# Optimization experiments

Hardware: AMD Instinct MI355X
Metric: run time of the kernel (lower is better)

Reference implementation:

```python
import jax, jax.numpy as jnp
import numpy as np

B, S, E, H = 4, 2048, 1024, 16
HD = E // H  # head_dim = 64


def setup_inputs() -> dict:
    key = jax.random.key(0)
    ks = jax.random.split(key, 9)
    s_in = 1.0 / np.sqrt(E)
    return {
        "x": jax.random.normal(ks[0], (B, S, E), dtype=jnp.float32),
        "Wq": jax.random.normal(ks[1], (E, E), dtype=jnp.float32) * s_in,
        "bq": jax.random.normal(ks[2], (E,), dtype=jnp.float32) * 0.01,
        "Wk": jax.random.normal(ks[3], (E, E), dtype=jnp.float32) * s_in,
        "bk": jax.random.normal(ks[4], (E,), dtype=jnp.float32) * 0.01,
        "Wv": jax.random.normal(ks[5], (E, E), dtype=jnp.float32) * s_in,
        "bv": jax.random.normal(ks[6], (E,), dtype=jnp.float32) * 0.01,
        "Wo": jax.random.normal(ks[7], (E, E), dtype=jnp.float32) * s_in,
        "bo": jax.random.normal(ks[8], (E,), dtype=jnp.float32) * 0.01,
    }


def reference(x, Wq, bq, Wk, bk, Wv, bv, Wo, bo):
    b, s, e = x.shape
    # fused QKV projections (equivalent to concatenated per-head linears)
    q = x @ Wq + bq  # [b, s, e]
    k = x @ Wk + bk
    v = x @ Wv + bv
    # split heads: [b, h, s, hd]
    def split(t):
        return t.reshape(b, s, H, HD).transpose(0, 2, 1, 3)
    q, k, v = split(q), split(k), split(v)
    scale = 1.0 / np.sqrt(HD)
    attn = jnp.einsum("bhqd,bhkd->bhqk", q, k) * scale  # [b, h, s, s]
    causal = jnp.tril(jnp.ones((s, s), dtype=bool))
    attn = jnp.where(causal[None, None], attn, -jnp.inf)
    attn = jax.nn.softmax(attn, axis=-1)
    y = jnp.einsum("bhqk,bhkd->bhqd", attn, v)  # [b, h, s, hd]
    y = y.transpose(0, 2, 1, 3).reshape(b, s, e)
    return y @ Wo + bo
```

## Files before the change

### kernel.cpp

```cpp
#include <hip/hip_runtime.h>
#include <hip/hip_bf16.h>

#define B_ 4
#define S_ 2048
#define E_ 1024
#define H_ 16
#define HD_ 64
#define QS 3072

typedef __attribute__((ext_vector_type(8))) short bf16x8;
typedef __attribute__((ext_vector_type(4))) float f32x4;

__device__ __forceinline__ float b2f(unsigned short u) {
    union { unsigned u; float f; } v; v.u = ((unsigned)u) << 16; return v.f;
}
__device__ __forceinline__ unsigned short f2b(float f) {
    union { float f; unsigned u; } v; v.f = f;
    unsigned lsb = (v.u >> 16) & 1u;
    v.u += 0x7fffu + lsb;
    return (unsigned short)(v.u >> 16);
}
__device__ __forceinline__ unsigned cvtpk_bf16(float lo, float hi) {
    unsigned r;
    asm("v_cvt_pk_bf16_f32 %0, %1, %2" : "=v"(r) : "v"(lo), "v"(hi));
    return r;
}

typedef const __attribute__((address_space(1))) unsigned glb_u32;
typedef __attribute__((address_space(3))) unsigned lds_u32;
__device__ __forceinline__ void gl_lds16(const unsigned short* g,
                                         unsigned short* l) {
    __builtin_amdgcn_global_load_lds((glb_u32*)g, (lds_u32*)l, 16, 0, 0);
}

__global__ void cvt_f32_to_bf16(const float* __restrict__ in,
                                unsigned short* __restrict__ out, int n8) {
    int i = blockIdx.x * blockDim.x + threadIdx.x;
    if (i >= n8) return;
    const float4* p = (const float4*)(in + (size_t)i * 8);
    float4 a = p[0], b = p[1];
    bf16x8 o;
    o[0] = (short)f2b(a.x); o[1] = (short)f2b(a.y);
    o[2] = (short)f2b(a.z); o[3] = (short)f2b(a.w);
    o[4] = (short)f2b(b.x); o[5] = (short)f2b(b.y);
    o[6] = (short)f2b(b.z); o[7] = (short)f2b(b.w);
    *(bf16x8*)(out + (size_t)i * 8) = o;
}

__global__ void transpose_cvt(const float* __restrict__ W,
                              unsigned short* __restrict__ Wt) {
    __shared__ float tile[32][33];
    int tx = threadIdx.x, ty = threadIdx.y;
    int x0 = blockIdx.x * 32, y0 = blockIdx.y * 32;
#pragma unroll
    for (int j = 0; j < 32; j += 8)
        tile[ty + j][tx] = W[(size_t)(y0 + ty + j) * E_ + x0 + tx];
    __syncthreads();
#pragma unroll
    for (int j = 0; j < 32; j += 8)
        Wt[(size_t)(x0 + ty + j) * E_ + y0 + tx] = f2b(tile[tx][ty + j]);
}

#define BM 128
#define BN 128
#define BK 32

__global__ __launch_bounds__(256) void gemm_bt(
        const unsigned short* __restrict__ A,
        const unsigned short* __restrict__ Bt,
        const float* __restrict__ b0, const float* __restrict__ b1,
        const float* __restrict__ b2,
        float* __restrict__ Cf, unsigned short* __restrict__ Cb,
        int M, int N, int K) {
    __shared__ unsigned short As[BM][BK];
    __shared__ unsigned short Bs[BN][BK];
    int t = threadIdx.x;
    int lane = t & 63, wid = t >> 6;
    int wr = wid >> 1, wc = wid & 1;
    int bx = blockIdx.x, by = blockIdx.y;
    const int row = t >> 2, kc = (t & 3) << 3;
    const unsigned short* ga0 = A + (size_t)(by * BM + row) * K + kc;
    const unsigned short* gb0 = Bt + (size_t)(bx * BN + row) * K + kc;
    unsigned short* la0 = &As[0][0] + (size_t)t * 8;
    unsigned short* lb0 = &Bs[0][0] + (size_t)t * 8;
    const size_t step64 = (size_t)64 * K;

    f32x4 acc[4][4] = {};

    for (int ko = 0; ko < K; ko += BK) {
        gl_lds16(ga0 + ko, la0);
        gl_lds16(ga0 + ko + step64, la0 + 2048);
        gl_lds16(gb0 + ko, lb0);
        gl_lds16(gb0 + ko + step64, lb0 + 2048);
        __syncthreads();
        int kg = (lane >> 4) << 3;
        bf16x8 af[4], bfr[4];
#pragma unroll
        for (int i = 0; i < 4; ++i) {
            af[i]  = *(const bf16x8*)&As[wr * 64 + i * 16 + (lane & 15)][kg];
            bfr[i] = *(const bf16x8*)&Bs[wc * 64 + i * 16 + (lane & 15)][kg];
        }
#pragma unroll
        for (int i = 0; i < 4; ++i)
#pragma unroll
            for (int j = 0; j < 4; ++j)
                acc[i][j] = __builtin_amdgcn_mfma_f32_16x16x32_bf16(
                    af[i], bfr[j], acc[i][j], 0, 0, 0);
        __syncthreads();
    }

#pragma unroll
    for (int i = 0; i < 4; ++i) {
        int row0 = by * BM + wr * 64 + i * 16 + ((lane >> 4) << 2);
#pragma unroll
        for (int j = 0; j < 4; ++j) {
            int col = bx * BN + wc * 64 + j * 16 + (lane & 15);
            const float* bp = (col < 1024) ? b0 : ((col < 2048) ? b1 : b2);
            float bv = bp[col & 1023];
#pragma unroll
            for (int r = 0; r < 4; ++r) {
                int rr = row0 + r;
                float v = acc[i][j][r] + bv;
                if (Cf) Cf[(size_t)rr * N + col] = v;
                else    Cb[(size_t)rr * N + col] = f2b(v);
            }
        }
    }
}

#define KVBLK 64

__global__ __launch_bounds__(256) void attn_mfma(
        const unsigned short* __restrict__ QKV,
        unsigned short* __restrict__ Yb) {
    __shared__ unsigned short Ks[KVBLK][64];
    __shared__ unsigned short Vt[64][KVBLK];
    __shared__ unsigned short Pl[4][32][64];

    int t = threadIdx.x;
    int lane = t & 63, wid = t >> 6;
    int l15 = lane & 15, lg = lane >> 4;
    int bh = blockIdx.x;
    int b = bh >> 4, h = bh & 15;
    int by = gridDim.y - 1 - blockIdx.y;
    int qbase = by * 128 + wid * 32;
    int vidx = lg << 4;

    const float qscale = 0.125f * 1.44269504f;
    bf16x8 qf[2][2];
#pragma unroll
    for (int mt = 0; mt < 2; ++mt)
#pragma unroll
        for (int ks = 0; ks < 2; ++ks) {
            int row = qbase + mt * 16 + l15;
            bf16x8 v = *(const bf16x8*)&QKV[((size_t)(b * S_ + row)) * QS +
                                            h * 64 + ks * 32 + lg * 8];
#pragma unroll
            for (int e = 0; e < 8; ++e)
                qf[mt][ks][e] = (short)f2b(b2f((unsigned short)v[e]) * qscale);
        }

    f32x4 yacc[2][4] = {};
    float m_[2] = {-1e30f, -1e30f}, l_[2] = {0.f, 0.f};

    int ntiles = by * 2 + 2;
    for (int kt = 0; kt < ntiles; ++kt) {
        int k0 = kt * KVBLK;
        __syncthreads();
        {
            int key = t >> 2;
            int c4 = (t & 3) * 16;
            size_t g = ((size_t)(b * S_ + k0 + key)) * QS + 1024 + h * 64 + c4;
            bf16x8 k0v = *(const bf16x8*)&QKV[g];
            bf16x8 k1v = *(const bf16x8*)&QKV[g + 8];
            bf16x8 v0v = *(const bf16x8*)&QKV[g + 1024];
            bf16x8 v1v = *(const bf16x8*)&QKV[g + 1032];
            int swk = (key & 7) << 3;
            *(bf16x8*)&Ks[key][c4 ^ swk] = k0v;
            *(bf16x8*)&Ks[key][(c4 + 8) ^ swk] = k1v;
#pragma unroll
            for (int e = 0; e < 8; ++e) {
                int d0 = c4 + e, d1 = c4 + 8 + e;
                int s0 = (d0 & 7) ^ ((d0 >> 3) & 7);
                int s1 = (d1 & 7) ^ ((d1 >> 3) & 7);
                Vt[d0][key ^ (s0 << 3)] = (unsigned short)v0v[e];
                Vt[d1][key ^ (s1 << 3)] = (unsigned short)v1v[e];
            }
        }
        __syncthreads();

        if (k0 <= qbase + 31) {
            bool boundary = (k0 + KVBLK - 1 > qbase);
            f32x4 sacc[2][4] = {};
#pragma unroll
            for (int ks = 0; ks < 2; ++ks) {
                bf16x8 kf[4];
#pragma unroll
                for (int n = 0; n < 4; ++n)
                    kf[n] = *(const bf16x8*)&Ks[n * 16 + l15]
                              [(ks * 32 + lg * 8) ^ ((l15 & 7) << 3)];
#pragma unroll
                for (int mt = 0; mt < 2; ++mt)
#pragma unroll
                    for (int n = 0; n < 4; ++n)
                        sacc[mt][n] = __builtin_amdgcn_mfma_f32_16x16x32_bf16(
                            kf[n], qf[mt][ks], sacc[mt][n], 0, 0, 0);
            }

#pragma unroll
            for (int mt = 0; mt < 2; ++mt) {
                int qv = qbase + mt * 16 + l15;
                if (boundary) {
#pragma unroll
                    for (int n = 0; n < 4; ++n)
#pragma unroll
                        for (int r = 0; r < 4; ++r)
                            if (k0 + n * 16 + lg * 4 + r > qv)
                                sacc[mt][n][r] = -3e38f;
                }
                float pm = -3e38f;
#pragma unroll
                for (int n = 0; n < 4; ++n)
#pragma unroll
                    for (int r = 0; r < 4; ++r)
                        pm = fmaxf(pm, sacc[mt][n][r]);
                pm = fmaxf(pm, __shfl_xor(pm, 16));
                pm = fmaxf(pm, __shfl_xor(pm, 32));
                float mn = fmaxf(m_[mt], pm);
                float corr = __builtin_exp2f(m_[mt] - mn);
                m_[mt] = mn;
                float rs = 0.f;
#pragma unroll
                for (int n = 0; n < 4; ++n)
#pragma unroll
                    for (int r = 0; r < 4; ++r) {
                        float p = __builtin_exp2f(sacc[mt][n][r] - mn);
                        sacc[mt][n][r] = p;
                        rs += p;
                    }
                rs += __shfl_xor(rs, 16);
                rs += __shfl_xor(rs, 32);
                l_[mt] = l_[mt] * corr + rs;
                int ci = __float_as_int(corr);
#pragma unroll
                for (int r = 0; r < 4; ++r) {
                    float cq = __int_as_float(
                        __builtin_amdgcn_ds_bpermute(vidx + 4 * r, ci));
#pragma unroll
                    for (int n = 0; n < 4; ++n) yacc[mt][n][r] *= cq;
                }
#pragma unroll
                for (int n = 0; n < 4; ++n)
#pragma unroll
                    for (int j = 0; j < 2; ++j) {
                        unsigned u = cvtpk_bf16(sacc[mt][n][2 * j],
                                                sacc[mt][n][2 * j + 1]);
                        int col = (n * 16 + lg * 4 + 2 * j) ^ ((l15 & 7) << 3);
                        *(unsigned*)&Pl[wid][mt * 16 + l15][col] = u;
                    }
            }
#pragma unroll
            for (int ks = 0; ks < 2; ++ks) {
                bf16x8 pa[2], vf[4];
#pragma unroll
                for (int mt = 0; mt < 2; ++mt)
                    pa[mt] = *(const bf16x8*)&Pl[wid][mt * 16 + l15]
                               [(ks * 32 + lg * 8) ^ ((l15 & 7) << 3)];
#pragma unroll
                for (int nd = 0; nd < 4; ++nd) {
                    int d = nd * 16 + l15;
                    int sig = (d & 7) ^ ((d >> 3) & 7);
                    vf[nd] = *(const bf16x8*)&Vt[d]
                               [(ks * 32 + lg * 8) ^ (sig << 3)];
                }
#pragma unroll
                for (int mt = 0; mt < 2; ++mt)
#pragma unroll
                    for (int nd = 0; nd < 4; ++nd)
                        yacc[mt][nd] = __builtin_amdgcn_mfma_f32_16x16x32_bf16(
                            pa[mt], vf[nd], yacc[mt][nd], 0, 0, 0);
            }
        }
    }

#pragma unroll
    for (int mt = 0; mt < 2; ++mt) {
        float inv = 1.f / l_[mt];
        int ii = __float_as_int(inv);
        float iv[4];
#pragma unroll
        for (int r = 0; r < 4; ++r)
            iv[r] = __int_as_float(
                __builtin_amdgcn_ds_bpermute(vidx + 4 * r, ii));
#pragma unroll
        for (int n = 0; n < 4; ++n)
#pragma unroll
            for (int r = 0; r < 4; ++r) {
                int row = qbase + mt * 16 + lg * 4 + r;
                int d = n * 16 + l15;
                Yb[((size_t)(b * S_ + row)) * E_ + h * 64 + d] =
                    f2b(yacc[mt][n][r] * iv[r]);
            }
    }
}

extern "C" void kernel_launch(void* const* d_in, const int* in_sizes, int n_in,
                              void* d_out, int out_size, void* d_ws, size_t ws_size,
                              hipStream_t stream) {
    const float* x  = (const float*)d_in[0];
    const float* Wq = (const float*)d_in[1];
    const float* bq = (const float*)d_in[2];
    const float* Wk = (const float*)d_in[3];
    const float* bk = (const float*)d_in[4];
    const float* Wv = (const float*)d_in[5];
    const float* bv = (const float*)d_in[6];
    const float* Wo = (const float*)d_in[7];
    const float* bo = (const float*)d_in[8];

    char* ws = (char*)d_ws;
    const size_t M = (size_t)B_ * S_;
    unsigned short* xb   = (unsigned short*)ws;
    unsigned short* QKVb = (unsigned short*)(ws + (16ull << 20));
    unsigned short* Wqkv = (unsigned short*)(ws + (64ull << 20));
    unsigned short* Wto  = (unsigned short*)(ws + (70ull << 20));
    unsigned short* Yb   = xb;

    int n8 = (int)(M * E_ / 8);
    cvt_f32_to_bf16<<<(n8 + 255) / 256, 256, 0, stream>>>(x, xb, n8);

    dim3 tb(32, 8), tg(32, 32);
    transpose_cvt<<<tg, tb, 0, stream>>>(Wq, Wqkv);
    transpose_cvt<<<tg, tb, 0, stream>>>(Wk, Wqkv + (size_t)1024 * E_);
    transpose_cvt<<<tg, tb, 0, stream>>>(Wv, Wqkv + (size_t)2048 * E_);
    transpose_cvt<<<tg, tb, 0, stream>>>(Wo, Wto);

    dim3 gq(QS / BN, M / BM);
    gemm_bt<<<gq, 256, 0, stream>>>(xb, Wqkv, bq, bk, bv, nullptr, QKVb,
                                    (int)M, QS, E_);

    dim3 ag(B_ * H_, S_ / 128);
    attn_mfma<<<ag, 256, 0, stream>>>(QKVb, Yb);

    dim3 gg(E_ / BN, M / BM);
    gemm_bt<<<gg, 256, 0, stream>>>(Yb, Wto, bo, bo, bo, (float*)d_out, nullptr,
                                    (int)M, E_, E_);
}
```

Baseline: 229.9 us.

## Pair causal query tiles per block and skip small softmax rescales

Each attention block now handles two query tiles, one short and one long (qt and NQT-1-qt), so causal work per block is balanced. The shared K/V tile loads are reused across both tiles. The grid is halved. Separately, the online-softmax rescale of the accumulator is skipped unless the new row max exceeds the old one by more than 8 (in log2 units), which removes exp and bpermute work in the common case. The cost is twice the per-thread accumulator and Q-fragment registers, which can lower occupancy. The lazy rescale lets probabilities grow up to 2^8 before renormalising, which may affect bf16 precision of P.

New measurement: 263.5 us. 14.6% more time.

```diff
diff --git a/kernel.cpp b/kernel.cpp
--- a/kernel.cpp
+++ b/kernel.cpp
@@ -142,28 +142,34 @@
     int l15 = lane & 15, lg = lane >> 4;
     int bh = blockIdx.x;
     int b = bh >> 4, h = bh & 15;
-    int by = gridDim.y - 1 - blockIdx.y;
-    int qbase = by * 128 + wid * 32;
+    const int NQT = S_ / 128;
+    int qt0 = blockIdx.y;
+    int qt1 = NQT - 1 - blockIdx.y;
+    int qb[2] = {qt0 * 128 + wid * 32, qt1 * 128 + wid * 32};
     int vidx = lg << 4;
 
     const float qscale = 0.125f * 1.44269504f;
-    bf16x8 qf[2][2];
-#pragma unroll
-    for (int mt = 0; mt < 2; ++mt)
-#pragma unroll
-        for (int ks = 0; ks < 2; ++ks) {
-            int row = qbase + mt * 16 + l15;
-            bf16x8 v = *(const bf16x8*)&QKV[((size_t)(b * S_ + row)) * QS +
-                                            h * 64 + ks * 32 + lg * 8];
-#pragma unroll
-            for (int e = 0; e < 8; ++e)
-                qf[mt][ks][e] = (short)f2b(b2f((unsigned short)v[e]) * qscale);
-        }
-
-    f32x4 yacc[2][4] = {};
-    float m_[2] = {-1e30f, -1e30f}, l_[2] = {0.f, 0.f};
-
-    int ntiles = by * 2 + 2;
+    bf16x8 qf[2][2][2];
+#pragma unroll
+    for (int s = 0; s < 2; ++s)
+#pragma unroll
+        for (int mt = 0; mt < 2; ++mt)
+#pragma unroll
+            for (int ks = 0; ks < 2; ++ks) {
+                int row = qb[s] + mt * 16 + l15;
+                bf16x8 v = *(const bf16x8*)&QKV[((size_t)(b * S_ + row)) * QS +
+                                                h * 64 + ks * 32 + lg * 8];
+#pragma unroll
+                for (int e = 0; e < 8; ++e)
+                    qf[s][mt][ks][e] =
+                        (short)f2b(b2f((unsigned short)v[e]) * qscale);
+            }
+
+    f32x4 yacc[2][2][4] = {};
+    float m_[2][2] = {{-1e30f, -1e30f}, {-1e30f, -1e30f}};
+    float l_[2][2] = {};
+
+    int ntiles = qt1 * 2 + 2;
     for (int kt = 0; kt < ntiles; ++kt) {
         int k0 = kt * KVBLK;
         __syncthreads();
@@ -189,8 +195,10 @@
         }
         __syncthreads();
 
-        if (k0 <= qbase + 31) {
-            bool boundary = (k0 + KVBLK - 1 > qbase);
+#pragma unroll
+        for (int s = 0; s < 2; ++s) {
+            if (k0 > qb[s] + 31) continue;
+            bool boundary = (k0 + KVBLK - 1 > qb[s]);
             f32x4 sacc[2][4] = {};
 #pragma unroll
             for (int ks = 0; ks < 2; ++ks) {
@@ -204,12 +212,12 @@
 #pragma unroll
                     for (int n = 0; n < 4; ++n)
                         sacc[mt][n] = __builtin_amdgcn_mfma_f32_16x16x32_bf16(
-                            kf[n], qf[mt][ks], sacc[mt][n], 0, 0, 0);
+                            kf[n], qf[s][mt][ks], sacc[mt][n], 0, 0, 0);
             }
 
 #pragma unroll
             for (int mt = 0; mt < 2; ++mt) {
-                int qv = qbase + mt * 16 + l15;
+                int qv = qb[s] + mt * 16 + l15;
                 if (boundary) {
 #pragma unroll
                     for (int n = 0; n < 4; ++n)
@@ -226,9 +234,23 @@
                         pm = fmaxf(pm, sacc[mt][n][r]);
                 pm = fmaxf(pm, __shfl_xor(pm, 16));
                 pm = fmaxf(pm, __shfl_xor(pm, 32));
-                float mn = fmaxf(m_[mt], pm);
-                float corr = __builtin_exp2f(m_[mt] - mn);
-                m_[mt] = mn;
+                float mo = m_[s][mt];
+                float mn = mo;
+                bool need = __any(pm > mo + 8.0f);
+                if (need) {
+                    mn = fmaxf(mo, pm);
+                    float corr = __builtin_exp2f(mo - mn);
+                    m_[s][mt] = mn;
+                    l_[s][mt] *= corr;
+                    int ci = __float_as_int(corr);
+#pragma unroll
+                    for (int r = 0; r < 4; ++r) {
+                        float cq = __int_as_float(
+                            __builtin_amdgcn_ds_bpermute(vidx + 4 * r, ci));
+#pragma unroll
+                        for (int n = 0; n < 4; ++n) yacc[s][mt][n][r] *= cq;
+                    }
+                }
                 float rs = 0.f;
 #pragma unroll
                 for (int n = 0; n < 4; ++n)
@@ -240,15 +262,7 @@
                     }
                 rs += __shfl_xor(rs, 16);
                 rs += __shfl_xor(rs, 32);
-                l_[mt] = l_[mt] * corr + rs;
-                int ci = __float_as_int(corr);
-#pragma unroll
-                for (int r = 0; r < 4; ++r) {
-                    float cq = __int_as_float(
-                        __builtin_amdgcn_ds_bpermute(vidx + 4 * r, ci));
-#pragma unroll
-                    for (int n = 0; n < 4; ++n) yacc[mt][n][r] *= cq;
-                }
+                l_[s][mt] += rs;
 #pragma unroll
                 for (int n = 0; n < 4; ++n)
 #pragma unroll
@@ -277,31 +291,33 @@
                 for (int mt = 0; mt < 2; ++mt)
 #pragma unroll
                     for (int nd = 0; nd < 4; ++nd)
-                        yacc[mt][nd] = __builtin_amdgcn_mfma_f32_16x16x32_bf16(
-                            pa[mt], vf[nd], yacc[mt][nd], 0, 0, 0);
+                        yacc[s][mt][nd] = __builtin_amdgcn_mfma_f32_16x16x32_bf16(
+                            pa[mt], vf[nd], yacc[s][mt][nd], 0, 0, 0);
             }
         }
     }
 
 #pragma unroll
-    for (int mt = 0; mt < 2; ++mt) {
-        float inv = 1.f / l_[mt];
-        int ii = __float_as_int(inv);
-        float iv[4];
-#pragma unroll
-        for (int r = 0; r < 4; ++r)
-            iv[r] = __int_as_float(
-                __builtin_amdgcn_ds_bpermute(vidx + 4 * r, ii));
-#pragma unroll
-        for (int n = 0; n < 4; ++n)
-#pragma unroll
-            for (int r = 0; r < 4; ++r) {
-                int row = qbase + mt * 16 + lg * 4 + r;
-                int d = n * 16 + l15;
-                Yb[((size_t)(b * S_ + row)) * E_ + h * 64 + d] =
-                    f2b(yacc[mt][n][r] * iv[r]);
-            }
-    }
+    for (int s = 0; s < 2; ++s)
+#pragma unroll
+        for (int mt = 0; mt < 2; ++mt) {
+            float inv = 1.f / l_[s][mt];
+            int ii = __float_as_int(inv);
+            float iv[4];
+#pragma unroll
+            for (int r = 0; r < 4; ++r)
+                iv[r] = __int_as_float(
+                    __builtin_amdgcn_ds_bpermute(vidx + 4 * r, ii));
+#pragma unroll
+            for (int n = 0; n < 4; ++n)
+#pragma unroll
+                for (int r = 0; r < 4; ++r) {
+                    int row = qb[s] + mt * 16 + lg * 4 + r;
+                    int d = n * 16 + l15;
+                    Yb[((size_t)(b * S_ + row)) * E_ + h * 64 + d] =
+                        f2b(yacc[s][mt][n][r] * iv[r]);
+                }
+        }
 }
 
 extern "C" void kernel_launch(void* const* d_in, const int* in_sizes, int n_in,
@@ -338,7 +354,7 @@
     gemm_bt<<<gq, 256, 0, stream>>>(xb, Wqkv, bq, bk, bv, nullptr, QKVb,
                                     (int)M, QS, E_);
 
-    dim3 ag(B_ * H_, S_ / 128);
+    dim3 ag(B_ * H_, S_ / 256);
     attn_mfma<<<ag, 256, 0, stream>>>(QKVb, Yb);
 
     dim3 gg(E_ / BN, M / BM);
```

## Double-buffer K/V tiles with async LDS loads and lazy softmax rescaling

Applied to the files above, without the earlier changes.

K and V tiles are now double-buffered in shared memory. The next tile's K is fetched with direct global-to-LDS loads and its V is held in registers while the current tile is computed, which removes one barrier per iteration and overlaps memory latency with MFMA work. Separately, the online softmax now rescales the running max and accumulators only when some new row max exceeds the old one by more than 8 (in log2 units). This skips the exp and bpermute rescaling on most tiles, at the cost of letting the unnormalized values grow by up to 2^8 in fp32/bf16. Shared memory use doubles for K/V, which may reduce occupancy.

Measured after the change: 222.6 us. 1.03x faster.

```diff
diff --git a/kernel.cpp b/kernel.cpp
--- a/kernel.cpp
+++ b/kernel.cpp
@@ -133,8 +133,8 @@
 __global__ __launch_bounds__(256) void attn_mfma(
         const unsigned short* __restrict__ QKV,
         unsigned short* __restrict__ Yb) {
-    __shared__ unsigned short Ks[KVBLK][64];
-    __shared__ unsigned short Vt[64][KVBLK];
+    __shared__ unsigned short Ks[2][KVBLK][64];
+    __shared__ unsigned short Vt[2][64][KVBLK];
     __shared__ unsigned short Pl[4][32][64];
 
     int t = threadIdx.x;
@@ -146,6 +146,13 @@
     int qbase = by * 128 + wid * 32;
     int vidx = lg << 4;
 
+    const int kk1 = t >> 3, kk2 = 32 + kk1;
+    const int kg1 = ((t & 7) ^ (kk1 & 7)) << 3;
+    const int kg2 = ((t & 7) ^ (kk2 & 7)) << 3;
+    const int vkey = t >> 2, vc4 = (t & 3) << 4;
+
+    const unsigned short* kvbase = QKV + ((size_t)b * S_) * QS + 1024 + h * 64;
+
     const float qscale = 0.125f * 1.44269504f;
     bf16x8 qf[2][2];
 #pragma unroll
@@ -164,30 +171,40 @@
     float m_[2] = {-1e30f, -1e30f}, l_[2] = {0.f, 0.f};
 
     int ntiles = by * 2 + 2;
+
+    {
+        gl_lds16(kvbase + (size_t)kk1 * QS + kg1, &Ks[0][0][0] + (size_t)t * 8);
+        gl_lds16(kvbase + (size_t)kk2 * QS + kg2,
+                 &Ks[0][0][0] + 2048 + (size_t)t * 8);
+        const unsigned short* vsrc = kvbase + 1024 + (size_t)vkey * QS + vc4;
+        bf16x8 v0 = *(const bf16x8*)vsrc;
+        bf16x8 v1 = *(const bf16x8*)(vsrc + 8);
+#pragma unroll
+        for (int e = 0; e < 8; ++e) {
+            int d0 = vc4 + e, d1 = vc4 + 8 + e;
+            int s0 = (d0 & 7) ^ ((d0 >> 3) & 7);
+            int s1 = (d1 & 7) ^ ((d1 >> 3) & 7);
+            Vt[0][d0][vkey ^ (s0 << 3)] = (unsigned short)v0[e];
+            Vt[0][d1][vkey ^ (s1 << 3)] = (unsigned short)v1[e];
+        }
+    }
+    __syncthreads();
+
+    int cur = 0;
     for (int kt = 0; kt < ntiles; ++kt) {
         int k0 = kt * KVBLK;
-        __syncthreads();
-        {
-            int key = t >> 2;
-            int c4 = (t & 3) * 16;
-            size_t g = ((size_t)(b * S_ + k0 + key)) * QS + 1024 + h * 64 + c4;
-            bf16x8 k0v = *(const bf16x8*)&QKV[g];
-            bf16x8 k1v = *(const bf16x8*)&QKV[g + 8];
-            bf16x8 v0v = *(const bf16x8*)&QKV[g + 1024];
-            bf16x8 v1v = *(const bf16x8*)&QKV[g + 1032];
-            int swk = (key & 7) << 3;
-            *(bf16x8*)&Ks[key][c4 ^ swk] = k0v;
-            *(bf16x8*)&Ks[key][(c4 + 8) ^ swk] = k1v;
-#pragma unroll
-            for (int e = 0; e < 8; ++e) {
-                int d0 = c4 + e, d1 = c4 + 8 + e;
-                int s0 = (d0 & 7) ^ ((d0 >> 3) & 7);
-                int s1 = (d1 & 7) ^ ((d1 >> 3) & 7);
-                Vt[d0][key ^ (s0 << 3)] = (unsigned short)v0v[e];
-                Vt[d1][key ^ (s1 << 3)] = (unsigned short)v1v[e];
-            }
-        }
-        __syncthreads();
+        bool pre = (kt + 1 < ntiles);
+        bf16x8 nv0, nv1;
+        if (pre) {
+            const unsigned short* kb = kvbase + (size_t)(k0 + KVBLK) * QS;
+            unsigned short* ld = &Ks[cur ^ 1][0][0];
+            gl_lds16(kb + (size_t)kk1 * QS + kg1, ld + (size_t)t * 8);
+            gl_lds16(kb + (size_t)kk2 * QS + kg2, ld + 2048 + (size_t)t * 8);
+            const unsigned short* vsrc =
+                kb + 1024 + (size_t)vkey * QS + vc4;
+            nv0 = *(const bf16x8*)vsrc;
+            nv1 = *(const bf16x8*)(vsrc + 8);
+        }
 
         if (k0 <= qbase + 31) {
             bool boundary = (k0 + KVBLK - 1 > qbase);
@@ -197,7 +214,7 @@
                 bf16x8 kf[4];
 #pragma unroll
                 for (int n = 0; n < 4; ++n)
-                    kf[n] = *(const bf16x8*)&Ks[n * 16 + l15]
+                    kf[n] = *(const bf16x8*)&Ks[cur][n * 16 + l15]
                               [(ks * 32 + lg * 8) ^ ((l15 & 7) << 3)];
 #pragma unroll
                 for (int mt = 0; mt < 2; ++mt)
@@ -226,9 +243,23 @@
                         pm = fmaxf(pm, sacc[mt][n][r]);
                 pm = fmaxf(pm, __shfl_xor(pm, 16));
                 pm = fmaxf(pm, __shfl_xor(pm, 32));
-                float mn = fmaxf(m_[mt], pm);
-                float corr = __builtin_exp2f(m_[mt] - mn);
-                m_[mt] = mn;
+                float mo = m_[mt];
+                float mn = mo;
+                bool need = __any(pm > mo + 8.0f);
+                if (need) {
+                    mn = fmaxf(mo, pm);
+                    float corr = __builtin_exp2f(mo - mn);
+                    m_[mt] = mn;
+                    l_[mt] *= corr;
+                    int ci = __float_as_int(corr);
+#pragma unroll
+                    for (int r = 0; r < 4; ++r) {
+                        float cq = __int_as_float(
+                            __builtin_amdgcn_ds_bpermute(vidx + 4 * r, ci));
+#pragma unroll
+                        for (int n = 0; n < 4; ++n) yacc[mt][n][r] *= cq;
+                    }
+                }
                 float rs = 0.f;
 #pragma unroll
                 for (int n = 0; n < 4; ++n)
@@ -240,15 +271,7 @@
                     }
                 rs += __shfl_xor(rs, 16);
                 rs += __shfl_xor(rs, 32);
-                l_[mt] = l_[mt] * corr + rs;
-                int ci = __float_as_int(corr);
-#pragma unroll
-                for (int r = 0; r < 4; ++r) {
-                    float cq = __int_as_float(
-                        __builtin_amdgcn_ds_bpermute(vidx + 4 * r, ci));
-#pragma unroll
-                    for (int n = 0; n < 4; ++n) yacc[mt][n][r] *= cq;
-                }
+                l_[mt] += rs;
 #pragma unroll
                 for (int n = 0; n < 4; ++n)
 #pragma unroll
@@ -270,7 +293,7 @@
                 for (int nd = 0; nd < 4; ++nd) {
                     int d = nd * 16 + l15;
                     int sig = (d & 7) ^ ((d >> 3) & 7);
-                    vf[nd] = *(const bf16x8*)&Vt[d]
+                    vf[nd] = *(const bf16x8*)&Vt[cur][d]
                                [(ks * 32 + lg * 8) ^ (sig << 3)];
                 }
 #pragma unroll
@@ -281,6 +304,19 @@
                             pa[mt], vf[nd], yacc[mt][nd], 0, 0, 0);
             }
         }
+
+        if (pre) {
+#pragma unroll
+            for (int e = 0; e < 8; ++e) {
+                int d0 = vc4 + e, d1 = vc4 + 8 + e;
+                int s0 = (d0 & 7) ^ ((d0 >> 3) & 7);
+                int s1 = (d1 & 7) ^ ((d1 >> 3) & 7);
+                Vt[cur ^ 1][d0][vkey ^ (s0 << 3)] = (unsigned short)nv0[e];
+                Vt[cur ^ 1][d1][vkey ^ (s1 << 3)] = (unsigned short)nv1[e];
+            }
+        }
+        __syncthreads();
+        cur ^= 1;
     }
 
 #pragma unroll
```
